# Optimization experiments

Measured on AMD Instinct MI355X. Metric: run time of the kernel, lower is better.

## Reference

```python
import jax, jax.numpy as jnp
import numpy as np

N = 8192

def setup_inputs() -> dict:
    key = jax.random.key(0)
    Graph_adj = jax.random.uniform(key, (N, N), dtype=jnp.float32)
    return {"Graph_adj": Graph_adj}

def reference(Graph_adj):
    # D = diag(1/sqrt(rowsum)), inf -> 0
    d = 1.0 / jnp.sqrt(jnp.sum(Graph_adj, axis=1))
    d = jnp.where(jnp.isinf(d), 0.0, d)
    # D @ A @ D expressed as broadcast row/col scaling (same math as diag-matmul chain)
    DAD = d[:, None] * Graph_adj * d[None, :]
    I = jnp.eye(Graph_adj.shape[0], dtype=Graph_adj.dtype)
    L = I - DAD            # normalized Laplacian
    Lfilter = I - L        # == DAD (low-pass filter)
    Hfilter = I + L        # == 2I - DAD (high-pass filter)
    return (Lfilter, Hfilter, Graph_adj)
```

## Files before the change

### kernel.cpp

```cpp
#include <hip/hip_runtime.h>

#define NN 8192

typedef float f32x4 __attribute__((ext_vector_type(4)));

__global__ __launch_bounds__(256) void rowsum_copy_kernel(
    const float* __restrict__ A, float* __restrict__ d, float* __restrict__ ga) {
    const int row = blockIdx.x;
    const f32x4* Arow = reinterpret_cast<const f32x4*>(A + (size_t)row * NN);
    f32x4*       Grow = reinterpret_cast<f32x4*>(ga + (size_t)row * NN);
    float s = 0.f;
    for (int k = threadIdx.x; k < NN / 4; k += 256) {
        f32x4 v = Arow[k];
        __builtin_nontemporal_store(v, &Grow[k]);
        s += (v.x + v.y) + (v.z + v.w);
    }
    #pragma unroll
    for (int off = 32; off > 0; off >>= 1)
        s += __shfl_down(s, off, 64);
    __shared__ float ls[4];
    const int lane = threadIdx.x & 63;
    const int wid  = threadIdx.x >> 6;
    if (lane == 0) ls[wid] = s;
    __syncthreads();
    if (threadIdx.x == 0) {
        float t = (ls[0] + ls[1]) + (ls[2] + ls[3]);
        d[row] = (t > 0.f) ? (1.0f / sqrtf(t)) : 0.f;
    }
}

__global__ __launch_bounds__(256) void build_filters_kernel(
    const float* __restrict__ A, const float* __restrict__ d,
    float* __restrict__ lf, float* __restrict__ hf, int nblocks) {
    const size_t idx = (size_t)(nblocks - 1 - blockIdx.x) * 256 + threadIdx.x;
    const int i  = (int)(idx >> 11);
    const int j4 = (int)(idx & 2047);
    const int j  = j4 * 4;

    f32x4 a  = reinterpret_cast<const f32x4*>(A)[idx];
    float di = d[i];
    f32x4 dj = reinterpret_cast<const f32x4*>(d)[j4];

    f32x4 dad = di * a * dj;

    f32x4 h;
    h.x = ((j + 0) == i ? 2.0f : 0.0f) - dad.x;
    h.y = ((j + 1) == i ? 2.0f : 0.0f) - dad.y;
    h.z = ((j + 2) == i ? 2.0f : 0.0f) - dad.z;
    h.w = ((j + 3) == i ? 2.0f : 0.0f) - dad.w;

    __builtin_nontemporal_store(dad, &reinterpret_cast<f32x4*>(lf)[idx]);
    __builtin_nontemporal_store(h,   &reinterpret_cast<f32x4*>(hf)[idx]);
}

extern "C" void kernel_launch(void* const* d_in, const int* in_sizes, int n_in,
                              void* d_out, int out_size, void* d_ws, size_t ws_size,
                              hipStream_t stream) {
    const float* A = (const float*)d_in[0];
    float* out = (float*)d_out;
    const size_t M = (size_t)NN * NN;
    float* lf = out;
    float* hf = out + M;
    float* ga = out + 2 * M;
    float* d  = (float*)d_ws;

    rowsum_copy_kernel<<<NN, 256, 0, stream>>>(A, d, ga);

    const int nblocks = (int)(M / 4 / 256);
    build_filters_kernel<<<nblocks, 256, 0, stream>>>(A, d, lf, hf, nblocks);
}
```

Baseline: 196.9 us.

## Move input copy into filter kernel and unroll rowsum loads

The rowsum kernel becomes read-only with eight vector loads issued up front per thread. The pass-through copy of the adjacency matrix now happens in the filter kernel, which already reads A. Each filter block also handles two vectors per thread and loads the row scale once per block. The goal is better memory-level parallelism and a better-balanced read/write mix, at the risk of making the second kernel more write-bound.

Result: faster. 192.1 us (-2.4%).

```diff
diff --git a/kernel.cpp b/kernel.cpp
--- a/kernel.cpp
+++ b/kernel.cpp
@@ -4,17 +4,18 @@
 
 typedef float f32x4 __attribute__((ext_vector_type(4)));
 
-__global__ __launch_bounds__(256) void rowsum_copy_kernel(
-    const float* __restrict__ A, float* __restrict__ d, float* __restrict__ ga) {
+__global__ __launch_bounds__(256) void rowsum_kernel(
+    const float* __restrict__ A, float* __restrict__ d) {
     const int row = blockIdx.x;
     const f32x4* Arow = reinterpret_cast<const f32x4*>(A + (size_t)row * NN);
-    f32x4*       Grow = reinterpret_cast<f32x4*>(ga + (size_t)row * NN);
+    f32x4 v[8];
+    #pragma unroll
+    for (int u = 0; u < 8; ++u)
+        v[u] = Arow[threadIdx.x + 256 * u];
     float s = 0.f;
-    for (int k = threadIdx.x; k < NN / 4; k += 256) {
-        f32x4 v = Arow[k];
-        __builtin_nontemporal_store(v, &Grow[k]);
-        s += (v.x + v.y) + (v.z + v.w);
-    }
+    #pragma unroll
+    for (int u = 0; u < 8; ++u)
+        s += (v[u].x + v[u].y) + (v[u].z + v[u].w);
     #pragma unroll
     for (int off = 32; off > 0; off >>= 1)
         s += __shfl_down(s, off, 64);
@@ -31,26 +32,46 @@
 
 __global__ __launch_bounds__(256) void build_filters_kernel(
     const float* __restrict__ A, const float* __restrict__ d,
-    float* __restrict__ lf, float* __restrict__ hf, int nblocks) {
-    const size_t idx = (size_t)(nblocks - 1 - blockIdx.x) * 256 + threadIdx.x;
-    const int i  = (int)(idx >> 11);
-    const int j4 = (int)(idx & 2047);
-    const int j  = j4 * 4;
+    float* __restrict__ lf, float* __restrict__ hf, float* __restrict__ ga,
+    int nblocks) {
+    const size_t base = (size_t)(nblocks - 1 - blockIdx.x) * 512;
+    const size_t idx0 = base + threadIdx.x;
+    const size_t idx1 = idx0 + 256;
+    const int i = (int)(base >> 11);
+    const float di = d[i];
 
-    f32x4 a  = reinterpret_cast<const f32x4*>(A)[idx];
-    float di = d[i];
-    f32x4 dj = reinterpret_cast<const f32x4*>(d)[j4];
+    const f32x4* A4 = reinterpret_cast<const f32x4*>(A);
+    const f32x4* d4 = reinterpret_cast<const f32x4*>(d);
 
-    f32x4 dad = di * a * dj;
+    f32x4 a0 = A4[idx0];
+    f32x4 a1 = A4[idx1];
+    f32x4 dj0 = d4[idx0 & 2047];
+    f32x4 dj1 = d4[idx1 & 2047];
 
-    f32x4 h;
-    h.x = ((j + 0) == i ? 2.0f : 0.0f) - dad.x;
-    h.y = ((j + 1) == i ? 2.0f : 0.0f) - dad.y;
-    h.z = ((j + 2) == i ? 2.0f : 0.0f) - dad.z;
-    h.w = ((j + 3) == i ? 2.0f : 0.0f) - dad.w;
+    f32x4 dad0 = di * a0 * dj0;
+    f32x4 dad1 = di * a1 * dj1;
 
-    __builtin_nontemporal_store(dad, &reinterpret_cast<f32x4*>(lf)[idx]);
-    __builtin_nontemporal_store(h,   &reinterpret_cast<f32x4*>(hf)[idx]);
+    const int j0 = (int)(idx0 & 2047) * 4;
+    const int j1 = (int)(idx1 & 2047) * 4;
+    f32x4 h0, h1;
+    h0.x = ((j0 + 0) == i ? 2.0f : 0.0f) - dad0.x;
+    h0.y = ((j0 + 1) == i ? 2.0f : 0.0f) - dad0.y;
+    h0.z = ((j0 + 2) == i ? 2.0f : 0.0f) - dad0.z;
+    h0.w = ((j0 + 3) == i ? 2.0f : 0.0f) - dad0.w;
+    h1.x = ((j1 + 0) == i ? 2.0f : 0.0f) - dad1.x;
+    h1.y = ((j1 + 1) == i ? 2.0f : 0.0f) - dad1.y;
+    h1.z = ((j1 + 2) == i ? 2.0f : 0.0f) - dad1.z;
+    h1.w = ((j1 + 3) == i ? 2.0f : 0.0f) - dad1.w;
+
+    f32x4* lf4 = reinterpret_cast<f32x4*>(lf);
+    f32x4* hf4 = reinterpret_cast<f32x4*>(hf);
+    f32x4* ga4 = reinterpret_cast<f32x4*>(ga);
+    __builtin_nontemporal_store(dad0, &lf4[idx0]);
+    __builtin_nontemporal_store(dad1, &lf4[idx1]);
+    __builtin_nontemporal_store(h0,   &hf4[idx0]);
+    __builtin_nontemporal_store(h1,   &hf4[idx1]);
+    __builtin_nontemporal_store(a0,   &ga4[idx0]);
+    __builtin_nontemporal_store(a1,   &ga4[idx1]);
 }
 
 extern "C" void kernel_launch(void* const* d_in, const int* in_sizes, int n_in,
@@ -64,8 +85,8 @@
     float* ga = out + 2 * M;
     float* d  = (float*)d_ws;
 
-    rowsum_copy_kernel<<<NN, 256, 0, stream>>>(A, d, ga);
+    rowsum_kernel<<<NN, 256, 0, stream>>>(A, d);
 
-    const int nblocks = (int)(M / 4 / 256);
-    build_filters_kernel<<<nblocks, 256, 0, stream>>>(A, d, lf, hf, nblocks);
+    const int nblocks = (int)(M / 4 / 512);
+    build_filters_kernel<<<nblocks, 256, 0, stream>>>(A, d, lf, hf, ga, nblocks);
 }
```
